# Kernel optimization log

Measured on AMD Instinct MI355X. Metric: run time of the kernel, lower is better.

The kernel has to match this reference:

```python
import jax, jax.numpy as jnp
from jax import lax
import numpy as np

N_ITER = 50  # entmax.EntmaxBisect default n_iter


def _p(z, alpha):
    # inverse of g'(t) = t**(alpha-1): clamp then fractional power
    return jnp.maximum(z, 0.0) ** (1.0 / (alpha - 1.0))


def entmax_bisect(x, alpha):
    """alpha-entmax over the last axis via 50-step bisection (entmax.EntmaxBisect)."""
    am1 = alpha - 1.0
    X = x * am1
    d = X.shape[-1]
    max_val = jnp.max(X, axis=-1, keepdims=True)
    tau_lo = max_val - 1.0                    # max - _gp(1, alpha)
    tau_hi = max_val - (1.0 / d) ** am1       # max - _gp(1/d, alpha)
    f_lo = jnp.sum(_p(X - tau_lo, alpha), axis=-1, keepdims=True) - 1.0
    dm0 = tau_hi - tau_lo

    def body(i, carry):
        dm, tlo, _ = carry
        dm = dm / 2.0
        tau_m = tlo + dm
        p_m = _p(X - tau_m, alpha)
        f_m = jnp.sum(p_m, axis=-1, keepdims=True) - 1.0
        mask = (f_m * f_lo) >= 0.0
        tlo = jnp.where(mask, tau_m, tlo)
        return dm, tlo, p_m

    _, _, p_m = lax.fori_loop(0, N_ITER, body, (dm0, tau_lo, jnp.zeros_like(X)))
    # ensure_sum_one=True
    return p_m / jnp.sum(p_m, axis=-1, keepdims=True)


def setup_inputs() -> dict:
    key = jax.random.key(0)
    in_value = jax.random.normal(key, (2048, 32000), dtype=jnp.float32)
    alpha = jnp.asarray(1.5, dtype=jnp.float32)  # the q parameter
    return {"in_value": in_value, "alpha": alpha}


def reference(in_value, alpha):
    return entmax_bisect(in_value, alpha)
```

## Files before the change

### kernel.cpp

```cpp
#include <hip/hip_runtime.h>
#include <math.h>


#define D_DIM   32000
#define NV4     (D_DIM / 4)
#define BLOCK   512
#define NWAVE   (BLOCK / 64)
#define GROUP   4
#define CAP     6144
#define NEWTON_MAX 30
#define NITER   50

__device__ __forceinline__ float wave_sum(float v) {
#pragma unroll
    for (int off = 32; off > 0; off >>= 1) v += __shfl_xor(v, off, 64);
    return v;
}
__device__ __forceinline__ float pf(float z, bool sq, float expo) {
    z = fmaxf(z, 0.0f);
    return sq ? z * z : powf(z, expo);
}
__device__ __forceinline__ unsigned fflip(float f) {
    unsigned u = __float_as_uint(f);
    return u ^ ((u >> 31) ? 0xFFFFFFFFu : 0x80000000u);
}
__device__ __forceinline__ float funflip(unsigned u) {
    return __uint_as_float(u ^ ((u & 0x80000000u) ? 0x80000000u : 0xFFFFFFFFu));
}

__global__ __launch_bounds__(BLOCK, 4)
void entmax_bisect_kernel(const float* __restrict__ x,
                          const float* __restrict__ alpha_p,
                          float* __restrict__ out) {
    const int row  = blockIdx.x;
    const int tid  = threadIdx.x;
    const int lane = tid & 63;
    const int wid  = tid >> 6;

    __shared__ float          s_val[CAP];
    __shared__ unsigned short s_idx[CAP];
    __shared__ float          s_red[NWAVE];
    __shared__ float          s_bc[2];
    __shared__ int            s_cnt;
    volatile __shared__ unsigned s_gmax;

    const float alpha = alpha_p[0];
    const float am1   = alpha - 1.0f;
    const float expo  = 1.0f / am1;
    const bool  sq    = (expo == 2.0f);

    const float4* __restrict__ x4 = (const float4*)(x + (size_t)row * D_DIM);
    float4*       __restrict__ o4 = (float4*)(out + (size_t)row * D_DIM);

    if (tid == 0) { s_cnt = 0; s_gmax = 0u; }
    __syncthreads();

    const float4 zero4 = make_float4(0.f, 0.f, 0.f, 0.f);
    float Xp[GROUP][4];
    int   pG0 = -1;

    for (int g0 = tid; g0 < NV4; g0 += GROUP * BLOCK) {
        float4 v[GROUP];
#pragma unroll
        for (int u = 0; u < GROUP; ++u) {
            const int i4 = g0 + u * BLOCK;
            if (i4 < NV4) {
                v[u] = x4[i4];
                o4[i4] = zero4;
            } else {
                v[u] = make_float4(-INFINITY, -INFINITY, -INFINITY, -INFINITY);
            }
        }
        float X[GROUP][4];
        float gm = -INFINITY;
#pragma unroll
        for (int u = 0; u < GROUP; ++u) {
            X[u][0] = v[u].x * am1; X[u][1] = v[u].y * am1;
            X[u][2] = v[u].z * am1; X[u][3] = v[u].w * am1;
            gm = fmaxf(gm, fmaxf(fmaxf(X[u][0], X[u][1]),
                                 fmaxf(X[u][2], X[u][3])));
        }
        unsigned r = s_gmax;
        const unsigned fm = fflip(gm);
        if (fm > r) { atomicMax((unsigned*)&s_gmax, fm); r = fm; }
        if (pG0 >= 0) {
            const float thr = funflip(r) - 1.0f;
            int cnt = 0;
            bool on[GROUP][4];
#pragma unroll
            for (int u = 0; u < GROUP; ++u)
#pragma unroll
                for (int c = 0; c < 4; ++c) {
                    on[u][c] = Xp[u][c] > thr;
                    cnt += (int)on[u][c];
                }
            if (cnt) {
                int base = atomicAdd(&s_cnt, cnt);
#pragma unroll
                for (int u = 0; u < GROUP; ++u)
#pragma unroll
                    for (int c = 0; c < 4; ++c)
                        if (on[u][c]) {
                            if (base < CAP) {
                                s_val[base] = Xp[u][c];
                                s_idx[base] = (unsigned short)((pG0 + u * BLOCK) * 4 + c);
                            }
                            ++base;
                        }
            }
        }
#pragma unroll
        for (int u = 0; u < GROUP; ++u)
#pragma unroll
            for (int c = 0; c < 4; ++c) Xp[u][c] = X[u][c];
        pG0 = g0;
    }
    if (pG0 >= 0) {
        const float thr = funflip((unsigned)s_gmax) - 1.0f;
        int cnt = 0;
        bool on[GROUP][4];
#pragma unroll
        for (int u = 0; u < GROUP; ++u)
#pragma unroll
            for (int c = 0; c < 4; ++c) {
                on[u][c] = Xp[u][c] > thr;
                cnt += (int)on[u][c];
            }
        if (cnt) {
            int base = atomicAdd(&s_cnt, cnt);
#pragma unroll
            for (int u = 0; u < GROUP; ++u)
#pragma unroll
                for (int c = 0; c < 4; ++c)
                    if (on[u][c]) {
                        if (base < CAP) {
                            s_val[base] = Xp[u][c];
                            s_idx[base] = (unsigned short)((pG0 + u * BLOCK) * 4 + c);
                        }
                        ++base;
                    }
        }
    }
    __syncthreads();
    const int   n_act   = s_cnt;
    const float max_val = funflip((unsigned)s_gmax);
    const float tau_lo0 = max_val - 1.0f;

    if (n_act <= CAP) {
        if (wid == 0) {
            float tau, S;
            if (sq) {
                tau = tau_lo0;
                for (int it = 0; it < NEWTON_MAX; ++it) {
                    float s1 = 0.f, s2 = 0.f;
                    for (int i = lane; i < n_act; i += 64) {
                        const float z = fmaxf(s_val[i] - tau, 0.f);
                        s1 += z; s2 += z * z;
                    }
#pragma unroll
                    for (int off = 32; off > 0; off >>= 1) {
                        s1 += __shfl_xor(s1, off, 64);
                        s2 += __shfl_xor(s2, off, 64);
                    }
                    const float dtau = (s2 - 1.0f) / fmaxf(2.0f * s1, 1e-30f);
                    tau += dtau;
                    if (dtau < 1e-7f * fmaxf(1.0f, fabsf(tau))) break;
                }
                float s2 = 0.f;
                for (int i = lane; i < n_act; i += 64) {
                    const float z = fmaxf(s_val[i] - tau, 0.f);
                    s2 += z * z;
                }
                S = wave_sum(s2);
            } else {
                const float tau_hi = max_val - powf(1.0f / (float)D_DIM, am1);
                float dm = tau_hi - tau_lo0;
                float s = 0.f;
                for (int i = lane; i < n_act; i += 64)
                    s += pf(s_val[i] - tau_lo0, sq, expo);
                s = wave_sum(s);
                const float f_lo = s - 1.0f;
                float tlo = tau_lo0, tau_m = tau_lo0, fsum = s;
                for (int it = 0; it < NITER; ++it) {
                    dm *= 0.5f;
                    tau_m = tlo + dm;
                    float t = 0.f;
                    for (int i = lane; i < n_act; i += 64)
                        t += pf(s_val[i] - tau_m, sq, expo);
                    t = wave_sum(t);
                    fsum = t;
                    if ((t - 1.0f) * f_lo >= 0.0f) tlo = tau_m;
                }
                tau = tau_m; S = fsum;
            }
            if (lane == 0) { s_bc[0] = tau; s_bc[1] = S; }
        }
        __syncthreads();

        const float tau_f = s_bc[0];
        const float invS  = 1.0f / s_bc[1];
        for (int i = tid; i < n_act; i += BLOCK) {
            const float z = fmaxf(s_val[i] - tau_f, 0.f);
            const float p = sq ? z * z : powf(z, expo);
            out[(size_t)row * D_DIM + s_idx[i]] = p * invS;
        }
    } else {
        const float tau_hi = max_val - powf(1.0f / (float)D_DIM, am1);
        float dm = tau_hi - tau_lo0;
        float s = 0.f;
        for (int i4 = tid; i4 < NV4; i4 += BLOCK) {
            float4 v = x4[i4];
            s += pf(v.x * am1 - tau_lo0, sq, expo) + pf(v.y * am1 - tau_lo0, sq, expo)
               + pf(v.z * am1 - tau_lo0, sq, expo) + pf(v.w * am1 - tau_lo0, sq, expo);
        }
        s = wave_sum(s);
        __syncthreads();
        if (lane == 0) s_red[wid] = s;
        __syncthreads();
        float tot = 0.f;
#pragma unroll
        for (int w = 0; w < NWAVE; ++w) tot += s_red[w];
        const float f_lo = tot - 1.0f;
        float tlo = tau_lo0, tau_m = tau_lo0, fsum = tot;
        for (int it = 0; it < NITER; ++it) {
            dm *= 0.5f;
            tau_m = tlo + dm;
            float t = 0.f;
            for (int i4 = tid; i4 < NV4; i4 += BLOCK) {
                float4 v = x4[i4];
                t += pf(v.x * am1 - tau_m, sq, expo) + pf(v.y * am1 - tau_m, sq, expo)
                   + pf(v.z * am1 - tau_m, sq, expo) + pf(v.w * am1 - tau_m, sq, expo);
            }
            t = wave_sum(t);
            __syncthreads();
            if (lane == 0) s_red[wid] = t;
            __syncthreads();
            float tt = 0.f;
#pragma unroll
            for (int w = 0; w < NWAVE; ++w) tt += s_red[w];
            fsum = tt;
            if ((tt - 1.0f) * f_lo >= 0.0f) tlo = tau_m;
        }
        const float invS = 1.0f / fsum;
        __syncthreads();
        for (int i4 = tid; i4 < NV4; i4 += BLOCK) {
            float4 v = x4[i4];
            float4 o;
            o.x = pf(v.x * am1 - tau_m, sq, expo) * invS;
            o.y = pf(v.y * am1 - tau_m, sq, expo) * invS;
            o.z = pf(v.z * am1 - tau_m, sq, expo) * invS;
            o.w = pf(v.w * am1 - tau_m, sq, expo) * invS;
            o4[i4] = o;
        }
    }
}

extern "C" void kernel_launch(void* const* d_in, const int* in_sizes, int n_in,
                              void* d_out, int out_size, void* d_ws, size_t ws_size,
                              hipStream_t stream) {
    const float* x       = (const float*)d_in[0];
    const float* alpha_p = (const float*)d_in[1];
    float* out           = (float*)d_out;
    const int rows       = in_sizes[0] / D_DIM;
    entmax_bisect_kernel<<<rows, BLOCK, 0, stream>>>(x, alpha_p, out);
}
```

Baseline: 483.3 us.

## Load whole row into registers, then filter candidates with wave-aggregated atomics

The streaming grouped loop is replaced by loading all 16 float4 chunks per thread into registers at once, then writing the zeros, then doing a single max/filter pass. The running max now uses a wave-level reduction with one atomic per wave, and the candidate slot is found with a wave prefix scan and one atomicAdd per wave. The threshold is compared in raw x-space to avoid multiplies. This raises memory-level parallelism and cuts shared-memory atomic traffic, at the cost of much higher register use, which is why launch bounds drop to 2 blocks per CU and occupancy falls. The threshold uses only the partial max seen so far, so more candidates may pass the filter.

```diff
diff --git a/kernel.cpp b/kernel.cpp
--- a/kernel.cpp
+++ b/kernel.cpp
@@ -6,7 +6,7 @@
 #define NV4     (D_DIM / 4)
 #define BLOCK   512
 #define NWAVE   (BLOCK / 64)
-#define GROUP   4
+#define NCHUNK  16
 #define CAP     6144
 #define NEWTON_MAX 30
 #define NITER   50
@@ -16,6 +16,11 @@
     for (int off = 32; off > 0; off >>= 1) v += __shfl_xor(v, off, 64);
     return v;
 }
+__device__ __forceinline__ float wave_max(float v) {
+#pragma unroll
+    for (int off = 32; off > 0; off >>= 1) v = fmaxf(v, __shfl_xor(v, off, 64));
+    return v;
+}
 __device__ __forceinline__ float pf(float z, bool sq, float expo) {
     z = fmaxf(z, 0.0f);
     return sq ? z * z : powf(z, expo);
@@ -28,7 +33,7 @@
     return __uint_as_float(u ^ ((u & 0x80000000u) ? 0x80000000u : 0xFFFFFFFFu));
 }
 
-__global__ __launch_bounds__(BLOCK, 4)
+__global__ __launch_bounds__(BLOCK, 2)
 void entmax_bisect_kernel(const float* __restrict__ x,
                           const float* __restrict__ alpha_p,
                           float* __restrict__ out) {
@@ -42,12 +47,13 @@
     __shared__ float          s_red[NWAVE];
     __shared__ float          s_bc[2];
     __shared__ int            s_cnt;
-    volatile __shared__ unsigned s_gmax;
-
-    const float alpha = alpha_p[0];
-    const float am1   = alpha - 1.0f;
-    const float expo  = 1.0f / am1;
-    const bool  sq    = (expo == 2.0f);
+    __shared__ unsigned       s_gmax;
+
+    const float alpha   = alpha_p[0];
+    const float am1     = alpha - 1.0f;
+    const float inv_am1 = 1.0f / am1;
+    const float expo    = inv_am1;
+    const bool  sq      = (expo == 2.0f);
 
     const float4* __restrict__ x4 = (const float4*)(x + (size_t)row * D_DIM);
     float4*       __restrict__ o4 = (float4*)(out + (size_t)row * D_DIM);
@@ -56,94 +62,70 @@
     __syncthreads();
 
     const float4 zero4 = make_float4(0.f, 0.f, 0.f, 0.f);
-    float Xp[GROUP][4];
-    int   pG0 = -1;
-
-    for (int g0 = tid; g0 < NV4; g0 += GROUP * BLOCK) {
-        float4 v[GROUP];
-#pragma unroll
-        for (int u = 0; u < GROUP; ++u) {
-            const int i4 = g0 + u * BLOCK;
-            if (i4 < NV4) {
-                v[u] = x4[i4];
-                o4[i4] = zero4;
-            } else {
-                v[u] = make_float4(-INFINITY, -INFINITY, -INFINITY, -INFINITY);
+    float4 v[NCHUNK];
+#pragma unroll
+    for (int k = 0; k < NCHUNK; ++k) {
+        const int i4 = tid + (k << 9);
+        if (i4 < NV4) v[k] = x4[i4];
+        else          v[k] = make_float4(-INFINITY, -INFINITY, -INFINITY, -INFINITY);
+    }
+    __builtin_amdgcn_sched_barrier(0);
+#pragma unroll
+    for (int k = 0; k < NCHUNK; ++k) {
+        const int i4 = tid + (k << 9);
+        if (i4 < NV4) o4[i4] = zero4;
+    }
+    __builtin_amdgcn_sched_barrier(0);
+
+    float tm = -INFINITY;
+#pragma unroll
+    for (int k = 0; k < NCHUNK; ++k)
+        tm = fmaxf(tm, fmaxf(fmaxf(v[k].x, v[k].y), fmaxf(v[k].z, v[k].w)));
+    const float wm  = wave_max(tm);
+    const float wmX = wm * am1;
+    if (lane == 0) atomicMax(&s_gmax, fflip(wmX));
+    const unsigned r = __hip_atomic_load(&s_gmax, __ATOMIC_RELAXED,
+                                         __HIP_MEMORY_SCOPE_WORKGROUP);
+    const float run   = fmaxf(funflip(r), wmX);
+    const float thr_x = (run - 1.0f) * inv_am1;
+
+    int cnt = 0;
+#pragma unroll
+    for (int k = 0; k < NCHUNK; ++k) {
+        cnt += (v[k].x > thr_x) + (v[k].y > thr_x)
+             + (v[k].z > thr_x) + (v[k].w > thr_x);
+    }
+    int inc = cnt;
+#pragma unroll
+    for (int off = 1; off < 64; off <<= 1) {
+        const int t = __shfl_up(inc, off, 64);
+        if (lane >= off) inc += t;
+    }
+    const int total = __shfl(inc, 63, 64);
+    if (total > 0) {
+        int base = 0;
+        if (lane == 63) base = atomicAdd(&s_cnt, total);
+        base = __shfl(base, 63, 64);
+        int pos = base + (inc - cnt);
+        auto append1 = [&](float val, int idx) {
+            if (val > thr_x) {
+                if (pos < CAP) {
+                    s_val[pos] = val * am1;
+                    s_idx[pos] = (unsigned short)idx;
+                }
+                ++pos;
             }
-        }
-        float X[GROUP][4];
-        float gm = -INFINITY;
-#pragma unroll
-        for (int u = 0; u < GROUP; ++u) {
-            X[u][0] = v[u].x * am1; X[u][1] = v[u].y * am1;
-            X[u][2] = v[u].z * am1; X[u][3] = v[u].w * am1;
-            gm = fmaxf(gm, fmaxf(fmaxf(X[u][0], X[u][1]),
-                                 fmaxf(X[u][2], X[u][3])));
-        }
-        unsigned r = s_gmax;
-        const unsigned fm = fflip(gm);
-        if (fm > r) { atomicMax((unsigned*)&s_gmax, fm); r = fm; }
-        if (pG0 >= 0) {
-            const float thr = funflip(r) - 1.0f;
-            int cnt = 0;
-            bool on[GROUP][4];
-#pragma unroll
-            for (int u = 0; u < GROUP; ++u)
-#pragma unroll
-                for (int c = 0; c < 4; ++c) {
-                    on[u][c] = Xp[u][c] > thr;
-                    cnt += (int)on[u][c];
-                }
-            if (cnt) {
-                int base = atomicAdd(&s_cnt, cnt);
-#pragma unroll
-                for (int u = 0; u < GROUP; ++u)
-#pragma unroll
-                    for (int c = 0; c < 4; ++c)
-                        if (on[u][c]) {
-                            if (base < CAP) {
-                                s_val[base] = Xp[u][c];
-                                s_idx[base] = (unsigned short)((pG0 + u * BLOCK) * 4 + c);
-                            }
-                            ++base;
-                        }
-            }
-        }
-#pragma unroll
-        for (int u = 0; u < GROUP; ++u)
-#pragma unroll
-            for (int c = 0; c < 4; ++c) Xp[u][c] = X[u][c];
-        pG0 = g0;
-    }
-    if (pG0 >= 0) {
-        const float thr = funflip((unsigned)s_gmax) - 1.0f;
-        int cnt = 0;
-        bool on[GROUP][4];
-#pragma unroll
-        for (int u = 0; u < GROUP; ++u)
-#pragma unroll
-            for (int c = 0; c < 4; ++c) {
-                on[u][c] = Xp[u][c] > thr;
-                cnt += (int)on[u][c];
-            }
-        if (cnt) {
-            int base = atomicAdd(&s_cnt, cnt);
-#pragma unroll
-            for (int u = 0; u < GROUP; ++u)
-#pragma unroll
-                for (int c = 0; c < 4; ++c)
-                    if (on[u][c]) {
-                        if (base < CAP) {
-                            s_val[base] = Xp[u][c];
-                            s_idx[base] = (unsigned short)((pG0 + u * BLOCK) * 4 + c);
-                        }
-                        ++base;
-                    }
+        };
+#pragma unroll
+        for (int k = 0; k < NCHUNK; ++k) {
+            const int e = (tid << 2) + k * 2048;
+            append1(v[k].x, e);     append1(v[k].y, e + 1);
+            append1(v[k].z, e + 2); append1(v[k].w, e + 3);
         }
     }
     __syncthreads();
     const int   n_act   = s_cnt;
-    const float max_val = funflip((unsigned)s_gmax);
+    const float max_val = funflip(s_gmax);
     const float tau_lo0 = max_val - 1.0f;
 
     if (n_act <= CAP) {
@@ -209,9 +191,9 @@
         float dm = tau_hi - tau_lo0;
         float s = 0.f;
         for (int i4 = tid; i4 < NV4; i4 += BLOCK) {
-            float4 v = x4[i4];
-            s += pf(v.x * am1 - tau_lo0, sq, expo) + pf(v.y * am1 - tau_lo0, sq, expo)
-               + pf(v.z * am1 - tau_lo0, sq, expo) + pf(v.w * am1 - tau_lo0, sq, expo);
+            float4 vv = x4[i4];
+            s += pf(vv.x * am1 - tau_lo0, sq, expo) + pf(vv.y * am1 - tau_lo0, sq, expo)
+               + pf(vv.z * am1 - tau_lo0, sq, expo) + pf(vv.w * am1 - tau_lo0, sq, expo);
         }
         s = wave_sum(s);
         __syncthreads();
@@ -227,9 +209,9 @@
             tau_m = tlo + dm;
             float t = 0.f;
             for (int i4 = tid; i4 < NV4; i4 += BLOCK) {
-                float4 v = x4[i4];
-                t += pf(v.x * am1 - tau_m, sq, expo) + pf(v.y * am1 - tau_m, sq, expo)
-                   + pf(v.z * am1 - tau_m, sq, expo) + pf(v.w * am1 - tau_m, sq, expo);
+                float4 vv = x4[i4];
+                t += pf(vv.x * am1 - tau_m, sq, expo) + pf(vv.y * am1 - tau_m, sq, expo)
+                   + pf(vv.z * am1 - tau_m, sq, expo) + pf(vv.w * am1 - tau_m, sq, expo);
             }
             t = wave_sum(t);
             __syncthreads();
@@ -244,12 +226,12 @@
         const float invS = 1.0f / fsum;
         __syncthreads();
         for (int i4 = tid; i4 < NV4; i4 += BLOCK) {
-            float4 v = x4[i4];
+            float4 vv = x4[i4];
             float4 o;
-            o.x = pf(v.x * am1 - tau_m, sq, expo) * invS;
-            o.y = pf(v.y * am1 - tau_m, sq, expo) * invS;
-            o.z = pf(v.z * am1 - tau_m, sq, expo) * invS;
-            o.w = pf(v.w * am1 - tau_m, sq, expo) * invS;
+            o.x = pf(vv.x * am1 - tau_m, sq, expo) * invS;
+            o.y = pf(vv.y * am1 - tau_m, sq, expo) * invS;
+            o.z = pf(vv.z * am1 - tau_m, sq, expo) * invS;
+            o.w = pf(vv.w * am1 - tau_m, sq, expo) * invS;
             o4[i4] = o;
         }
     }
```

Result: faster. 470.5 us (-2.6%).

## Split row max into a separate pass and compact candidates with exact threshold

Applied to the files above, without the earlier changes.

Adds a first kernel that computes each row's max and min, so the second kernel knows the exact threshold before compaction. This removes the speculative previous-group threshold and the shared-memory atomicMax. Compaction now uses a wave prefix scan with one atomic per wave, and small active sets are solved from registers rather than shared memory. The cost is a second full read of the input, an extra launch, and a smaller candidate capacity (CAP 4096), so rows with more candidates fall back to the slow full-row path sooner.

```diff
diff --git a/kernel.cpp b/kernel.cpp
--- a/kernel.cpp
+++ b/kernel.cpp
@@ -3,11 +3,16 @@
 
 
 #define D_DIM   32000
-#define NV4     (D_DIM / 4)
-#define BLOCK   512
-#define NWAVE   (BLOCK / 64)
-#define GROUP   4
-#define CAP     6144
+#define NV4     8000
+
+#define B1      256
+#define K1CH    32
+
+#define B2      512
+#define NWAVE2  8
+#define K2CH    16
+#define CAP     4096
+#define NCREG   16
 #define NEWTON_MAX 30
 #define NITER   50
 
@@ -20,135 +25,182 @@
     z = fmaxf(z, 0.0f);
     return sq ? z * z : powf(z, expo);
 }
-__device__ __forceinline__ unsigned fflip(float f) {
-    unsigned u = __float_as_uint(f);
-    return u ^ ((u >> 31) ? 0xFFFFFFFFu : 0x80000000u);
-}
-__device__ __forceinline__ float funflip(unsigned u) {
-    return __uint_as_float(u ^ ((u & 0x80000000u) ? 0x80000000u : 0xFFFFFFFFu));
-}
-
-__global__ __launch_bounds__(BLOCK, 4)
-void entmax_bisect_kernel(const float* __restrict__ x,
-                          const float* __restrict__ alpha_p,
-                          float* __restrict__ out) {
+__device__ __forceinline__ void block_sync_lds() {
+    asm volatile("s_waitcnt lgkmcnt(0)" ::: "memory");
+    __builtin_amdgcn_s_barrier();
+    asm volatile("" ::: "memory");
+}
+
+__global__ __launch_bounds__(B1, 8)
+void row_minmax_kernel(const float* __restrict__ x,
+                       float* __restrict__ ws_max,
+                       float* __restrict__ ws_min) {
     const int row  = blockIdx.x;
     const int tid  = threadIdx.x;
     const int lane = tid & 63;
     const int wid  = tid >> 6;
+    const float4* __restrict__ x4 = (const float4*)(x + (size_t)row * D_DIM);
+
+    float mx = -INFINITY, mn = INFINITY;
+#pragma unroll
+    for (int k = 0; k < K1CH; ++k) {
+        const int i4 = tid + (k << 8);
+        if (i4 < NV4) {
+            const float4 v = x4[i4];
+            mx = fmaxf(mx, fmaxf(fmaxf(v.x, v.y), fmaxf(v.z, v.w)));
+            mn = fminf(mn, fminf(fminf(v.x, v.y), fminf(v.z, v.w)));
+        }
+    }
+#pragma unroll
+    for (int off = 32; off > 0; off >>= 1) {
+        mx = fmaxf(mx, __shfl_xor(mx, off, 64));
+        mn = fminf(mn, __shfl_xor(mn, off, 64));
+    }
+    __shared__ float smx[B1 / 64], smn[B1 / 64];
+    if (lane == 0) { smx[wid] = mx; smn[wid] = mn; }
+    __syncthreads();
+    if (tid == 0) {
+        float a = smx[0], b = smn[0];
+#pragma unroll
+        for (int w = 1; w < B1 / 64; ++w) {
+            a = fmaxf(a, smx[w]); b = fminf(b, smn[w]);
+        }
+        ws_max[row] = a; ws_min[row] = b;
+    }
+}
+
+__global__ __launch_bounds__(B2, 4)
+void solve_apply_kernel(const float* __restrict__ x,
+                        const float* __restrict__ alpha_p,
+                        const float* __restrict__ ws_max,
+                        const float* __restrict__ ws_min,
+                        float* __restrict__ out) {
+    const int row  = blockIdx.x;
+    const int tid  = threadIdx.x;
+    const int lane = tid & 63;
 
     __shared__ float          s_val[CAP];
     __shared__ unsigned short s_idx[CAP];
-    __shared__ float          s_red[NWAVE];
-    __shared__ float          s_bc[2];
+    __shared__ float          s_red[NWAVE2];
     __shared__ int            s_cnt;
-    volatile __shared__ unsigned s_gmax;
 
     const float alpha = alpha_p[0];
     const float am1   = alpha - 1.0f;
     const float expo  = 1.0f / am1;
     const bool  sq    = (expo == 2.0f);
 
+    const float maxX    = (am1 >= 0.0f) ? am1 * ws_max[row] : am1 * ws_min[row];
+    const float tau_lo0 = maxX - 1.0f;
+
     const float4* __restrict__ x4 = (const float4*)(x + (size_t)row * D_DIM);
     float4*       __restrict__ o4 = (float4*)(out + (size_t)row * D_DIM);
-
-    if (tid == 0) { s_cnt = 0; s_gmax = 0u; }
+    float*        __restrict__ orow = out + (size_t)row * D_DIM;
+
+    if (tid == 0) s_cnt = 0;
     __syncthreads();
 
     const float4 zero4 = make_float4(0.f, 0.f, 0.f, 0.f);
-    float Xp[GROUP][4];
-    int   pG0 = -1;
-
-    for (int g0 = tid; g0 < NV4; g0 += GROUP * BLOCK) {
-        float4 v[GROUP];
-#pragma unroll
-        for (int u = 0; u < GROUP; ++u) {
-            const int i4 = g0 + u * BLOCK;
-            if (i4 < NV4) {
-                v[u] = x4[i4];
-                o4[i4] = zero4;
+    for (int k = 0; k < K2CH; ++k) {
+        const int i4 = tid + (k << 9);
+        float  X[4];
+        bool   on[4];
+        int    cnt = 0;
+        if (i4 < NV4) {
+            const float4 v = x4[i4];
+            X[0] = v.x * am1; X[1] = v.y * am1;
+            X[2] = v.z * am1; X[3] = v.w * am1;
+#pragma unroll
+            for (int c = 0; c < 4; ++c) {
+                on[c] = X[c] > tau_lo0;
+                cnt += (int)on[c];
+            }
+            o4[i4] = zero4;
+        } else {
+#pragma unroll
+            for (int c = 0; c < 4; ++c) on[c] = false;
+        }
+        int inc = cnt;
+#pragma unroll
+        for (int off = 1; off < 64; off <<= 1) {
+            const int t = __shfl_up(inc, off, 64);
+            if (lane >= off) inc += t;
+        }
+        const int wtotal = __shfl(inc, 63, 64);
+        if (wtotal > 0) {
+            int base = 0;
+            if (lane == 63) base = atomicAdd(&s_cnt, wtotal);
+            base = __shfl(base, 63, 64);
+            int pos = base + (inc - cnt);
+#pragma unroll
+            for (int c = 0; c < 4; ++c)
+                if (on[c]) {
+                    if (pos < CAP) {
+                        s_val[pos] = X[c];
+                        s_idx[pos] = (unsigned short)(i4 * 4 + c);
+                    }
+                    ++pos;
+                }
+        }
+    }
+    block_sync_lds();
+    const int n_act = s_cnt;
+
+    if (n_act <= CAP) {
+        float tau, S;
+        if (n_act <= NCREG * 64) {
+            float c[NCREG];
+#pragma unroll
+            for (int j = 0; j < NCREG; ++j) {
+                const int idx = (j << 6) + lane;
+                c[j] = (idx < n_act) ? s_val[idx] : -INFINITY;
+            }
+            if (sq) {
+                tau = tau_lo0;
+                for (int it = 0; it < NEWTON_MAX; ++it) {
+                    float s1 = 0.f, s2 = 0.f;
+#pragma unroll
+                    for (int j = 0; j < NCREG; ++j) {
+                        const float z = fmaxf(c[j] - tau, 0.f);
+                        s1 += z; s2 += z * z;
+                    }
+#pragma unroll
+                    for (int off = 32; off > 0; off >>= 1) {
+                        s1 += __shfl_xor(s1, off, 64);
+                        s2 += __shfl_xor(s2, off, 64);
+                    }
+                    const float dtau = (s2 - 1.0f) / fmaxf(2.0f * s1, 1e-30f);
+                    tau += dtau;
+                    if (dtau < 1e-7f * fmaxf(1.0f, fabsf(tau))) break;
+                }
+                float s2 = 0.f;
+#pragma unroll
+                for (int j = 0; j < NCREG; ++j) {
+                    const float z = fmaxf(c[j] - tau, 0.f);
+                    s2 += z * z;
+                }
+                S = wave_sum(s2);
             } else {
-                v[u] = make_float4(-INFINITY, -INFINITY, -INFINITY, -INFINITY);
-            }
-        }
-        float X[GROUP][4];
-        float gm = -INFINITY;
-#pragma unroll
-        for (int u = 0; u < GROUP; ++u) {
-            X[u][0] = v[u].x * am1; X[u][1] = v[u].y * am1;
-            X[u][2] = v[u].z * am1; X[u][3] = v[u].w * am1;
-            gm = fmaxf(gm, fmaxf(fmaxf(X[u][0], X[u][1]),
-                                 fmaxf(X[u][2], X[u][3])));
-        }
-        unsigned r = s_gmax;
-        const unsigned fm = fflip(gm);
-        if (fm > r) { atomicMax((unsigned*)&s_gmax, fm); r = fm; }
-        if (pG0 >= 0) {
-            const float thr = funflip(r) - 1.0f;
-            int cnt = 0;
-            bool on[GROUP][4];
-#pragma unroll
-            for (int u = 0; u < GROUP; ++u)
-#pragma unroll
-                for (int c = 0; c < 4; ++c) {
-                    on[u][c] = Xp[u][c] > thr;
-                    cnt += (int)on[u][c];
-                }
-            if (cnt) {
-                int base = atomicAdd(&s_cnt, cnt);
-#pragma unroll
-                for (int u = 0; u < GROUP; ++u)
-#pragma unroll
-                    for (int c = 0; c < 4; ++c)
-                        if (on[u][c]) {
-                            if (base < CAP) {
-                                s_val[base] = Xp[u][c];
-                                s_idx[base] = (unsigned short)((pG0 + u * BLOCK) * 4 + c);
-                            }
-                            ++base;
-                        }
-            }
-        }
-#pragma unroll
-        for (int u = 0; u < GROUP; ++u)
-#pragma unroll
-            for (int c = 0; c < 4; ++c) Xp[u][c] = X[u][c];
-        pG0 = g0;
-    }
-    if (pG0 >= 0) {
-        const float thr = funflip((unsigned)s_gmax) - 1.0f;
-        int cnt = 0;
-        bool on[GROUP][4];
-#pragma unroll
-        for (int u = 0; u < GROUP; ++u)
-#pragma unroll
-            for (int c = 0; c < 4; ++c) {
-                on[u][c] = Xp[u][c] > thr;
-                cnt += (int)on[u][c];
-            }
-        if (cnt) {
-            int base = atomicAdd(&s_cnt, cnt);
-#pragma unroll
-            for (int u = 0; u < GROUP; ++u)
-#pragma unroll
-                for (int c = 0; c < 4; ++c)
-                    if (on[u][c]) {
-                        if (base < CAP) {
-                            s_val[base] = Xp[u][c];
-                            s_idx[base] = (unsigned short)((pG0 + u * BLOCK) * 4 + c);
-                        }
-                        ++base;
-                    }
-        }
-    }
-    __syncthreads();
-    const int   n_act   = s_cnt;
-    const float max_val = funflip((unsigned)s_gmax);
-    const float tau_lo0 = max_val - 1.0f;
-
-    if (n_act <= CAP) {
-        if (wid == 0) {
-            float tau, S;
+                const float tau_hi = maxX - powf(1.0f / (float)D_DIM, am1);
+                float dm = tau_hi - tau_lo0;
+                float s = 0.f;
+#pragma unroll
+                for (int j = 0; j < NCREG; ++j) s += pf(c[j] - tau_lo0, sq, expo);
+                s = wave_sum(s);
+                const float f_lo = s - 1.0f;
+                float tlo = tau_lo0, tau_m = tau_lo0, fsum = s;
+                for (int it = 0; it < NITER; ++it) {
+                    dm *= 0.5f;
+                    tau_m = tlo + dm;
+                    float t = 0.f;
+#pragma unroll
+                    for (int j = 0; j < NCREG; ++j) t += pf(c[j] - tau_m, sq, expo);
+                    t = wave_sum(t);
+                    fsum = t;
+                    if ((t - 1.0f) * f_lo >= 0.0f) tlo = tau_m;
+                }
+                tau = tau_m; S = fsum;
+            }
+        } else {
             if (sq) {
                 tau = tau_lo0;
                 for (int it = 0; it < NEWTON_MAX; ++it) {
@@ -173,7 +225,7 @@
                 }
                 S = wave_sum(s2);
             } else {
-                const float tau_hi = max_val - powf(1.0f / (float)D_DIM, am1);
+                const float tau_hi = maxX - powf(1.0f / (float)D_DIM, am1);
                 float dm = tau_hi - tau_lo0;
                 float s = 0.f;
                 for (int i = lane; i < n_act; i += 64)
@@ -193,41 +245,40 @@
                 }
                 tau = tau_m; S = fsum;
             }
-            if (lane == 0) { s_bc[0] = tau; s_bc[1] = S; }
         }
         __syncthreads();
 
-        const float tau_f = s_bc[0];
-        const float invS  = 1.0f / s_bc[1];
-        for (int i = tid; i < n_act; i += BLOCK) {
-            const float z = fmaxf(s_val[i] - tau_f, 0.f);
+        const float invS = 1.0f / S;
+        for (int i = tid; i < n_act; i += B2) {
+            const float z = fmaxf(s_val[i] - tau, 0.f);
             const float p = sq ? z * z : powf(z, expo);
-            out[(size_t)row * D_DIM + s_idx[i]] = p * invS;
+            orow[s_idx[i]] = p * invS;
         }
     } else {
-        const float tau_hi = max_val - powf(1.0f / (float)D_DIM, am1);
+        const float tau_hi = maxX - powf(1.0f / (float)D_DIM, am1);
         float dm = tau_hi - tau_lo0;
         float s = 0.f;
-        for (int i4 = tid; i4 < NV4; i4 += BLOCK) {
-            float4 v = x4[i4];
+        for (int i4 = tid; i4 < NV4; i4 += B2) {
+            const float4 v = x4[i4];
             s += pf(v.x * am1 - tau_lo0, sq, expo) + pf(v.y * am1 - tau_lo0, sq, expo)
                + pf(v.z * am1 - tau_lo0, sq, expo) + pf(v.w * am1 - tau_lo0, sq, expo);
         }
         s = wave_sum(s);
+        const int wid = tid >> 6;
         __syncthreads();
         if (lane == 0) s_red[wid] = s;
         __syncthreads();
         float tot = 0.f;
 #pragma unroll
-        for (int w = 0; w < NWAVE; ++w) tot += s_red[w];
+        for (int w = 0; w < NWAVE2; ++w) tot += s_red[w];
         const float f_lo = tot - 1.0f;
         float tlo = tau_lo0, tau_m = tau_lo0, fsum = tot;
         for (int it = 0; it < NITER; ++it) {
             dm *= 0.5f;
             tau_m = tlo + dm;
             float t = 0.f;
-            for (int i4 = tid; i4 < NV4; i4 += BLOCK) {
-                float4 v = x4[i4];
+            for (int i4 = tid; i4 < NV4; i4 += B2) {
+                const float4 v = x4[i4];
                 t += pf(v.x * am1 - tau_m, sq, expo) + pf(v.y * am1 - tau_m, sq, expo)
                    + pf(v.z * am1 - tau_m, sq, expo) + pf(v.w * am1 - tau_m, sq, expo);
             }
@@ -237,14 +288,14 @@
             __syncthreads();
             float tt = 0.f;
 #pragma unroll
-            for (int w = 0; w < NWAVE; ++w) tt += s_red[w];
+            for (int w = 0; w < NWAVE2; ++w) tt += s_red[w];
             fsum = tt;
             if ((tt - 1.0f) * f_lo >= 0.0f) tlo = tau_m;
         }
         const float invS = 1.0f / fsum;
         __syncthreads();
-        for (int i4 = tid; i4 < NV4; i4 += BLOCK) {
-            float4 v = x4[i4];
+        for (int i4 = tid; i4 < NV4; i4 += B2) {
+            const float4 v = x4[i4];
             float4 o;
             o.x = pf(v.x * am1 - tau_m, sq, expo) * invS;
             o.y = pf(v.y * am1 - tau_m, sq, expo) * invS;
@@ -262,5 +313,9 @@
     const float* alpha_p = (const float*)d_in[1];
     float* out           = (float*)d_out;
     const int rows       = in_sizes[0] / D_DIM;
-    entmax_bisect_kernel<<<rows, BLOCK, 0, stream>>>(x, alpha_p, out);
-}
+    float* ws_max        = (float*)d_ws;
+    float* ws_min        = ws_max + rows;
+
+    row_minmax_kernel<<<rows, B1, 0, stream>>>(x, ws_max, ws_min);
+    solve_apply_kernel<<<rows, B2, 0, stream>>>(x, alpha_p, ws_max, ws_min, out);
+}
```

Result: slower. 539.1 us (+11.5%).
